# Performance work log

Hardware: AMD Instinct MI355X
Metric: run time of the kernel (lower is better)

The kernel has to match this reference:

```python
import jax, jax.numpy as jnp
import numpy as np

B, NS, S, H = 2048, 8, 8, 512   # batch, num_units, num_mem_slots, hidden==num_mem_size
WH, WK = 1, 32                  # write attention heads, key_size
RH, RK = 4, 32                  # read (mem) attention heads, mem_attention_key


def _lin(x, W, b):
    # torch nn.Linear convention: W is [out, in]
    return jnp.einsum('...i,oi->...o', x, W) + b


def setup_inputs() -> dict:
    key = jax.random.key(0)
    ks = jax.random.split(key, 13)
    def w(k, o, i):
        return jax.random.normal(k, (o, i), jnp.float32) * 0.02
    d = {
        'h_s': jax.random.normal(ks[0], (B, NS, H), jnp.float32),
        'mem': jax.random.normal(ks[1], (B, S, H), jnp.float32),
        'wq_w': w(ks[2], WH * WK, H), 'wq_b': jnp.zeros((WH * WK,), jnp.float32),
        'wk_w': w(ks[3], WH * WK, H), 'wk_b': jnp.zeros((WH * WK,), jnp.float32),
        'wv_w': w(ks[4], WH * H, H), 'wv_b': jnp.zeros((WH * H,), jnp.float32),
        'wo_w': w(ks[5], H, WH * H), 'wo_b': jnp.zeros((H,), jnp.float32),
        'ut_w': w(ks[6], H, H),      'ut_b': jnp.zeros((H,), jnp.float32),
        'ug_w': w(ks[7], 2 * H, H),  'ug_b': jnp.zeros((2 * H,), jnp.float32),
        'rq_w': w(ks[8], RH * RK, H), 'rq_b': jnp.zeros((RH * RK,), jnp.float32),
        'rk_w': w(ks[9], RH * RK, H), 'rk_b': jnp.zeros((RH * RK,), jnp.float32),
        'rv_w': w(ks[10], RH * H, H), 'rv_b': jnp.zeros((RH * H,), jnp.float32),
        'ro_w': w(ks[11], H, RH * H), 'ro_b': jnp.zeros((H,), jnp.float32),
    }
    return d


def _forward(h_s, mem, wq_w, wq_b, wk_w, wk_b, wv_w, wv_b, wo_w, wo_b,
             ut_w, ut_b, ug_w, ug_b, rq_w, rq_b, rk_w, rk_b, rv_w, rv_b,
             ro_w, ro_b):
    b = h_s.shape[0]
    T = NS + S  # concat length for write keys/values

    # ---------------- write ----------------
    xi = jnp.concatenate([h_s, mem], axis=1)                       # [B, T, H]
    q = _lin(mem, wq_w, wq_b).reshape(b, S, WH, WK).transpose(0, 2, 1, 3)   # [B,WH,S,WK]
    k = _lin(xi, wk_w, wk_b).reshape(b, T, WH, WK).transpose(0, 2, 1, 3)    # [B,WH,T,WK]
    v = _lin(xi, wv_w, wv_b).reshape(b, T, WH, H).transpose(0, 2, 1, 3)     # [B,WH,T,H]
    scores = jnp.einsum('bhsk,bhtk->bhst', q, k) / np.sqrt(WK).astype(np.float32)
    probs = jax.nn.softmax(scores, axis=-1)                         # [B,WH,S,T]
    ctx = jnp.einsum('bhst,bhtd->bhsd', probs, v)                   # [B,WH,S,H]
    ctx = ctx.transpose(0, 2, 1, 3).reshape(b, S, WH * H)
    mem_write = _lin(ctx, wo_w, wo_b)                               # [B,S,H]

    # ---------------- update (GRU-like gating) ----------------
    inputs_mean = jax.nn.relu(_lin(h_s, ut_w, ut_b)).mean(axis=1, keepdims=True)  # [B,1,H]
    kk = inputs_mean + jnp.tanh(mem)                                # [B,S,H]
    gates = jax.nn.sigmoid(_lin(kk, ug_w, ug_b))                    # [B,S,2H]
    input_gate, forget_gate = gates[..., :H], gates[..., H:]
    mem_new = input_gate * jnp.tanh(mem_write) + forget_gate * mem  # [B,S,H]

    # ---------------- read ----------------
    q = _lin(h_s, rq_w, rq_b).reshape(b, NS, RH, RK).transpose(0, 2, 1, 3)      # [B,RH,NS,RK]
    k = _lin(mem_new, rk_w, rk_b).reshape(b, S, RH, RK).transpose(0, 2, 1, 3)   # [B,RH,S,RK]
    v = _lin(mem_new, rv_w, rv_b).reshape(b, S, RH, H).transpose(0, 2, 1, 3)    # [B,RH,S,H]
    scores = jnp.einsum('bhnk,bhsk->bhns', q, k) / np.sqrt(RK).astype(np.float32)
    probs = jax.nn.softmax(scores, axis=-1)                          # [B,RH,NS,S]
    ctx = jnp.einsum('bhns,bhsd->bhnd', probs, v)                    # [B,RH,NS,H]
    ctx = ctx.transpose(0, 2, 1, 3).reshape(b, NS, RH * H)
    h_out = h_s + _lin(ctx, ro_w, ro_b)                              # residual
    return h_out, mem_new


def reference(h_s, mem, wq_w, wq_b, wk_w, wk_b, wv_w, wv_b, wo_w, wo_b,
              ut_w, ut_b, ug_w, ug_b, rq_w, rq_b, rk_w, rk_b, rv_w, rv_b,
              ro_w, ro_b):
    return _forward(h_s, mem, wq_w, wq_b, wk_w, wk_b, wv_w, wv_b, wo_w, wo_b,
                    ut_w, ut_b, ug_w, ug_b, rq_w, rq_b, rk_w, rk_b, rv_w, rv_b,
                    ro_w, ro_b)
```

## Files before the change

### kernel.cpp

```cpp
#include <hip/hip_runtime.h>

#define Bb   2048
#define Mrows 16384
#define Hd   512

typedef float  f32x4  __attribute__((ext_vector_type(4)));
typedef __bf16 bf16x8 __attribute__((ext_vector_type(8)));
typedef unsigned short us8 __attribute__((ext_vector_type(8)));

__device__ __forceinline__ unsigned short f2bf(float f) {
    unsigned int u = __builtin_bit_cast(unsigned int, f);
    u = u + 0x7FFFu + ((u >> 16) & 1u);
    return (unsigned short)(u >> 16);
}
__device__ __forceinline__ float bf2f(unsigned short h) {
    unsigned int u = ((unsigned int)h) << 16;
    return __builtin_bit_cast(float, u);
}

__device__ __forceinline__ void gload_lds16(const unsigned short* g, void* lds) {
    __builtin_amdgcn_global_load_lds(
        (const __attribute__((address_space(1))) unsigned int*)g,
        (__attribute__((address_space(3))) unsigned int*)lds,
        16, 0, 0);
}

#define MB (1024ull*1024ull)
#define OFF_WQ   0ull
#define OFF_WK   32768ull
#define OFF_WV   65536ull
#define OFF_WO   589824ull
#define OFF_UT   1114112ull
#define OFF_UG   1638400ull
#define OFF_RQ   2686976ull
#define OFF_RK   2818048ull
#define OFF_RV   2949120ull
#define OFF_RO   5046272ull
#define OFF_HS    (8*MB)
#define OFF_MEM   (24*MB)
#define OFF_UTR   (40*MB)
#define OFF_MEAN  (56*MB)
#define OFF_Q1    (60*MB)
#define OFF_K1    (62*MB)
#define OFF_V1    (66*MB)
#define OFF_CTX1  (100*MB)
#define OFF_KK    (116*MB)
#define OFF_TMW   (132*MB)
#define OFF_GATES (148*MB)
#define OFF_MNB   (180*MB)
#define OFF_Q2    (196*MB)
#define OFF_K2    (204*MB)
#define OFF_RVO   (40*MB)
#define OFF_CTX2  (104*MB)

struct CastSeg { const float* src; unsigned short* dst; int n4; };
struct CastParams { CastSeg seg[12]; };

__global__ __launch_bounds__(256) void cast_all(CastParams p) {
    CastSeg s = p.seg[blockIdx.y];
    int stride = gridDim.x * blockDim.x;
    for (int i = blockIdx.x * blockDim.x + threadIdx.x; i < s.n4; i += stride) {
        float4 v = reinterpret_cast<const float4*>(s.src)[i];
        ushort4 o;
        o.x = f2bf(v.x); o.y = f2bf(v.y); o.z = f2bf(v.z); o.w = f2bf(v.w);
        reinterpret_cast<ushort4*>(s.dst)[i] = o;
    }
}

template<int MODE>
__device__ __forceinline__ void store_c(void* out, const float* extra, int row,
                                        int col, int ldo, int remap_off, float v) {
    if (MODE == 0) {
        ((float*)out)[(size_t)row * ldo + col] = v;
    } else if (MODE == 1) {
        ((unsigned short*)out)[(size_t)row * ldo + col] = f2bf(v);
    } else if (MODE == 2) {
        ((unsigned short*)out)[(size_t)row * ldo + col] = f2bf(fmaxf(v, 0.f));
    } else if (MODE == 3) {
        ((unsigned short*)out)[(size_t)row * ldo + col] = f2bf(1.f / (1.f + expf(-v)));
    } else if (MODE == 4) {
        ((unsigned short*)out)[(size_t)row * ldo + col] = f2bf(tanhf(v));
    } else if (MODE == 5) {
        int rr = ((row >> 3) << 4) + (row & 7) + remap_off;
        ((float*)out)[(size_t)rr * ldo + col] = v;
    } else if (MODE == 6) {
        int rr = ((row >> 3) << 4) + (row & 7) + remap_off;
        ((unsigned short*)out)[(size_t)rr * ldo + col] = f2bf(v);
    } else if (MODE == 7) {
        ((float*)out)[(size_t)row * ldo + col] = v + extra[(size_t)row * ldo + col];
    }
}

struct GemmSeg {
    const unsigned short* A;
    const unsigned short* W;
    const float* bias;
    void* out;
    const float* extra;
    int mode, ldo, remap_off, tile0;
};
struct GemmParams { GemmSeg seg[4]; int nseg; int tiles_tot; };

template<int K>
__global__ __launch_bounds__(256, 2) void gemm_multi(GemmParams p)
{
    constexpr int NT = K / 64;
    __shared__ __align__(16) unsigned short As[2][128 * 64];
    __shared__ __align__(16) unsigned short Bs[2][128 * 64];

    const int nwg = (int)gridDim.x;
    const int swz = ((int)blockIdx.x & 7) * (nwg >> 3) + ((int)blockIdx.x >> 3);
    const int bm = swz / p.tiles_tot;
    const int tl = swz - bm * p.tiles_tot;

    int si = 0;
    #pragma unroll
    for (int i = 1; i < 4; i++)
        if (i < p.nseg && tl >= p.seg[i].tile0) si = i;
    const unsigned short* Aseg = p.seg[si].A;
    const unsigned short* Wseg = p.seg[si].W;
    const int bn = tl - p.seg[si].tile0;

    const int t = threadIdx.x;
    const int wave = t >> 6, lane = t & 63;
    const int wr = (wave >> 1) * 64;
    const int wc = (wave & 1) * 64;
    const int lrow = lane & 15;
    const int lkh  = lane >> 4;

    const unsigned short* ga[4];
    const unsigned short* gb[4];
    #pragma unroll
    for (int j = 0; j < 4; j++) {
        int c   = wave * 256 + j * 64 + lane;
        int row = c >> 3;
        int kl  = (c & 7) ^ (row & 7);
        ga[j] = Aseg + (size_t)(bm * 128 + row) * K + kl * 8;
        gb[j] = Wseg + (size_t)(bn * 128 + row) * K + kl * 8;
    }

    int aof[4][2], bof[4][2];
    #pragma unroll
    for (int m = 0; m < 4; m++) {
        int ra = wr + m * 16 + lrow;
        int rb = wc + m * 16 + lrow;
        #pragma unroll
        for (int kk = 0; kk < 2; kk++) {
            int kc = kk * 4 + lkh;
            aof[m][kk] = ra * 64 + ((kc ^ (ra & 7)) << 3);
            bof[m][kk] = rb * 64 + ((kc ^ (rb & 7)) << 3);
        }
    }

    f32x4 acc[4][4] = {};

    #pragma unroll
    for (int j = 0; j < 4; j++) {
        gload_lds16(ga[j], (char*)As[0] + (wave * 4 + j) * 1024);
        gload_lds16(gb[j], (char*)Bs[0] + (wave * 4 + j) * 1024);
    }
    __syncthreads();

    #pragma unroll 8
    for (int kt = 0; kt < NT; ++kt) {
        const int cur = kt & 1, nxt = cur ^ 1;
        if (kt + 1 < NT) {
            #pragma unroll
            for (int j = 0; j < 4; j++) {
                gload_lds16(ga[j] + (kt + 1) * 64, (char*)As[nxt] + (wave * 4 + j) * 1024);
                gload_lds16(gb[j] + (kt + 1) * 64, (char*)Bs[nxt] + (wave * 4 + j) * 1024);
            }
        }
        #pragma unroll
        for (int kk = 0; kk < 2; kk++) {
            bf16x8 af[4], bf_[4];
            #pragma unroll
            for (int m = 0; m < 4; m++)
                af[m] = __builtin_bit_cast(bf16x8,
                            *reinterpret_cast<const us8*>(&As[cur][aof[m][kk]]));
            #pragma unroll
            for (int n = 0; n < 4; n++)
                bf_[n] = __builtin_bit_cast(bf16x8,
                            *reinterpret_cast<const us8*>(&Bs[cur][bof[n][kk]]));
            #pragma unroll
            for (int m = 0; m < 4; m++)
                #pragma unroll
                for (int n = 0; n < 4; n++)
                    acc[m][n] = __builtin_amdgcn_mfma_f32_16x16x32_bf16(
                                    af[m], bf_[n], acc[m][n], 0, 0, 0);
        }
        __syncthreads();
    }

    void* outp = p.seg[si].out;
    const float* bias = p.seg[si].bias;
    const float* extra = p.seg[si].extra;
    const int ldo = p.seg[si].ldo, rmo = p.seg[si].remap_off, mode = p.seg[si].mode;

    #define EPI(MODE_)                                                          \
        _Pragma("unroll")                                                       \
        for (int n = 0; n < 4; n++) {                                           \
            int col = bn * 128 + wc + n * 16 + lrow;                            \
            float bv = bias[col];                                               \
            _Pragma("unroll")                                                   \
            for (int m = 0; m < 4; m++) {                                       \
                _Pragma("unroll")                                               \
                for (int r = 0; r < 4; r++) {                                   \
                    int row = bm * 128 + wr + m * 16 + lkh * 4 + r;             \
                    store_c<MODE_>(outp, extra, row, col, ldo, rmo,             \
                                   acc[m][n][r] + bv);                          \
                }                                                               \
            }                                                                   \
        }
    switch (mode) {
        case 0: EPI(0) break;
        case 1: EPI(1) break;
        case 2: EPI(2) break;
        case 3: EPI(3) break;
        case 4: EPI(4) break;
        case 5: EPI(5) break;
        case 6: EPI(6) break;
        default: EPI(7) break;
    }
    #undef EPI
}

template<int TN, int MODE, int K>
__global__ __launch_bounds__(256) void gemm_small(
    const unsigned short* __restrict__ A, const unsigned short* __restrict__ W,
    const float* __restrict__ bias, void* __restrict__ out,
    const float* __restrict__ extra, int N, int ldo, int remap_off)
{
    constexpr int BN = 16 * TN;
    const int tiles_n = N / BN;
    const int bm = blockIdx.x / tiles_n;
    const int bn = blockIdx.x % tiles_n;
    const int wave = threadIdx.x >> 6;
    const int lane = threadIdx.x & 63;
    const int row0 = bm * 64 + wave * 16;
    const int col0 = bn * BN;
    const int lrow = lane & 15;
    const int lk   = (lane >> 4) << 3;

    f32x4 acc[TN] = {};
    const unsigned short* ap  = A + (size_t)(row0 + lrow) * K + lk;
    const unsigned short* wp0 = W + (size_t)(col0 + lrow) * K + lk;

    #pragma unroll 4
    for (int ks = 0; ks < K; ks += 32) {
        bf16x8 af = __builtin_bit_cast(bf16x8,
                        *reinterpret_cast<const us8*>(ap + ks));
        #pragma unroll
        for (int tt = 0; tt < TN; tt++) {
            bf16x8 bfm = __builtin_bit_cast(bf16x8,
                        *reinterpret_cast<const us8*>(wp0 + (size_t)tt * 16 * K + ks));
            acc[tt] = __builtin_amdgcn_mfma_f32_16x16x32_bf16(af, bfm, acc[tt], 0, 0, 0);
        }
    }

    #pragma unroll
    for (int tt = 0; tt < TN; tt++) {
        int col = col0 + tt * 16 + lrow;
        float bv = bias[col];
        #pragma unroll
        for (int r = 0; r < 4; r++) {
            int row = row0 + (lane >> 4) * 4 + r;
            store_c<MODE>(out, extra, row, col, ldo, remap_off, acc[tt][r] + bv);
        }
    }
}

__global__ __launch_bounds__(256) void mean_kernel(
    const unsigned short* __restrict__ UTR, float* __restrict__ MEAN)
{
    int idx = blockIdx.x * blockDim.x + threadIdx.x;
    if (idx >= Bb * Hd) return;
    int b = idx >> 9, j = idx & 511;
    float s = 0.f;
    #pragma unroll
    for (int r = 0; r < 8; r++)
        s += bf2f(UTR[((size_t)(b * 8 + r) << 9) + j]);
    MEAN[idx] = s * 0.125f;
}

__global__ __launch_bounds__(256) void kk_kernel(
    const float* __restrict__ MEAN, const float* __restrict__ mem,
    unsigned short* __restrict__ KK)
{
    int idx = blockIdx.x * blockDim.x + threadIdx.x;
    int m = idx >> 9;
    int bj = ((m >> 3) << 9) + (idx & 511);
    KK[idx] = f2bf(MEAN[bj] + tanhf(mem[idx]));
}

__global__ __launch_bounds__(256) void memnew_kernel(
    const unsigned short* __restrict__ GATES, const unsigned short* __restrict__ TMW,
    const float* __restrict__ mem, float* __restrict__ out_mem,
    unsigned short* __restrict__ MNB)
{
    int idx = blockIdx.x * blockDim.x + threadIdx.x;
    int m = idx >> 9, j = idx & 511;
    float ig = bf2f(GATES[(size_t)m * 1024 + j]);
    float fg = bf2f(GATES[(size_t)m * 1024 + 512 + j]);
    float v  = ig * bf2f(TMW[idx]) + fg * mem[idx];
    out_mem[idx] = v;
    MNB[idx] = f2bf(v);
}

__global__ __launch_bounds__(256) void attn1_kernel(
    const float* __restrict__ Q1, const float* __restrict__ K1,
    const unsigned short* __restrict__ V1, unsigned short* __restrict__ CTX1)
{
    int b = blockIdx.x, t = threadIdx.x;
    __shared__ float q[8][32], k[16][32], pr[8][16];
    q[t >> 5][t & 31] = Q1[(size_t)b * 256 + t];
    k[t >> 5][t & 31]       = K1[(size_t)b * 512 + t];
    k[8 + (t >> 5)][t & 31] = K1[(size_t)b * 512 + 256 + t];
    __syncthreads();
    if (t < 128) {
        int s = t >> 4, tt = t & 15;
        float acc = 0.f;
        #pragma unroll
        for (int i = 0; i < 32; i++) acc += q[s][i] * k[tt][i];
        pr[s][tt] = acc * 0.17677669529663687f;
    }
    __syncthreads();
    if (t < 8) {
        float m = -1e30f;
        for (int i = 0; i < 16; i++) m = fmaxf(m, pr[t][i]);
        float e[16], sum = 0.f;
        for (int i = 0; i < 16; i++) { e[i] = expf(pr[t][i] - m); sum += e[i]; }
        float inv = 1.f / sum;
        for (int i = 0; i < 16; i++) pr[t][i] = e[i] * inv;
    }
    __syncthreads();
    int s = t >> 5, d0 = (t & 31) * 16;
    float a[16];
    #pragma unroll
    for (int i = 0; i < 16; i++) a[i] = 0.f;
    for (int tt = 0; tt < 16; tt++) {
        float p = pr[s][tt];
        const unsigned short* vp = V1 + ((size_t)(b * 16 + tt)) * 512 + d0;
        us8 v0 = *reinterpret_cast<const us8*>(vp);
        us8 v1 = *reinterpret_cast<const us8*>(vp + 8);
        #pragma unroll
        for (int i = 0; i < 8; i++) a[i]     += p * bf2f(v0[i]);
        #pragma unroll
        for (int i = 0; i < 8; i++) a[8 + i] += p * bf2f(v1[i]);
    }
    us8 o0, o1;
    #pragma unroll
    for (int i = 0; i < 8; i++) { o0[i] = f2bf(a[i]); o1[i] = f2bf(a[8 + i]); }
    unsigned short* cp = CTX1 + ((size_t)(b * 8 + s)) * 512 + d0;
    *reinterpret_cast<us8*>(cp) = o0;
    *reinterpret_cast<us8*>(cp + 8) = o1;
}

__global__ __launch_bounds__(256) void attn2_kernel(
    const float* __restrict__ Q2, const float* __restrict__ K2,
    const unsigned short* __restrict__ V2, unsigned short* __restrict__ CTX2)
{
    int b = blockIdx.x, t = threadIdx.x;
    __shared__ float q[8][128], k[8][128], pr[4][8][8];
    for (int i = t; i < 1024; i += 256) {
        q[i >> 7][i & 127] = Q2[(size_t)b * 1024 + i];
        k[i >> 7][i & 127] = K2[(size_t)b * 1024 + i];
    }
    __syncthreads();
    {
        int h = t >> 6, n = (t >> 3) & 7, s = t & 7;
        float acc = 0.f;
        #pragma unroll
        for (int i = 0; i < 32; i++) acc += q[n][h * 32 + i] * k[s][h * 32 + i];
        pr[h][n][s] = acc * 0.17677669529663687f;
    }
    __syncthreads();
    if (t < 32) {
        int h = t >> 3, n = t & 7;
        float m = -1e30f;
        for (int i = 0; i < 8; i++) m = fmaxf(m, pr[h][n][i]);
        float e[8], sum = 0.f;
        for (int i = 0; i < 8; i++) { e[i] = expf(pr[h][n][i] - m); sum += e[i]; }
        float inv = 1.f / sum;
        for (int i = 0; i < 8; i++) pr[h][n][i] = e[i] * inv;
    }
    __syncthreads();
    int n = t >> 5, d0 = (t & 31) * 16;
    for (int h = 0; h < 4; h++) {
        float a[16];
        #pragma unroll
        for (int i = 0; i < 16; i++) a[i] = 0.f;
        for (int s = 0; s < 8; s++) {
            float p = pr[h][n][s];
            const unsigned short* vp = V2 + ((size_t)(b * 8 + s)) * 2048 + h * 512 + d0;
            us8 v0 = *reinterpret_cast<const us8*>(vp);
            us8 v1 = *reinterpret_cast<const us8*>(vp + 8);
            #pragma unroll
            for (int i = 0; i < 8; i++) a[i]     += p * bf2f(v0[i]);
            #pragma unroll
            for (int i = 0; i < 8; i++) a[8 + i] += p * bf2f(v1[i]);
        }
        us8 o0, o1;
        #pragma unroll
        for (int i = 0; i < 8; i++) { o0[i] = f2bf(a[i]); o1[i] = f2bf(a[8 + i]); }
        unsigned short* cp = CTX2 + ((size_t)(b * 8 + n)) * 2048 + h * 512 + d0;
        *reinterpret_cast<us8*>(cp) = o0;
        *reinterpret_cast<us8*>(cp + 8) = o1;
    }
}

extern "C" void kernel_launch(void* const* d_in, const int* in_sizes, int n_in,
                              void* d_out, int out_size, void* d_ws, size_t ws_size,
                              hipStream_t stream)
{
    const float* h_s  = (const float*)d_in[0];
    const float* mem  = (const float*)d_in[1];
    const float* wq_w = (const float*)d_in[2];  const float* wq_b = (const float*)d_in[3];
    const float* wk_w = (const float*)d_in[4];  const float* wk_b = (const float*)d_in[5];
    const float* wv_w = (const float*)d_in[6];  const float* wv_b = (const float*)d_in[7];
    const float* wo_w = (const float*)d_in[8];  const float* wo_b = (const float*)d_in[9];
    const float* ut_w = (const float*)d_in[10]; const float* ut_b = (const float*)d_in[11];
    const float* ug_w = (const float*)d_in[12]; const float* ug_b = (const float*)d_in[13];
    const float* rq_w = (const float*)d_in[14]; const float* rq_b = (const float*)d_in[15];
    const float* rk_w = (const float*)d_in[16]; const float* rk_b = (const float*)d_in[17];
    const float* rv_w = (const float*)d_in[18]; const float* rv_b = (const float*)d_in[19];
    const float* ro_w = (const float*)d_in[20]; const float* ro_b = (const float*)d_in[21];

    char* ws = (char*)d_ws;
    unsigned short* WQb = (unsigned short*)(ws + OFF_WQ);
    unsigned short* WKb = (unsigned short*)(ws + OFF_WK);
    unsigned short* WVb = (unsigned short*)(ws + OFF_WV);
    unsigned short* WOb = (unsigned short*)(ws + OFF_WO);
    unsigned short* UTb = (unsigned short*)(ws + OFF_UT);
    unsigned short* UGb = (unsigned short*)(ws + OFF_UG);
    unsigned short* RQb = (unsigned short*)(ws + OFF_RQ);
    unsigned short* RKb = (unsigned short*)(ws + OFF_RK);
    unsigned short* RVb = (unsigned short*)(ws + OFF_RV);
    unsigned short* ROb = (unsigned short*)(ws + OFF_RO);
    unsigned short* HSb  = (unsigned short*)(ws + OFF_HS);
    unsigned short* MEMb = (unsigned short*)(ws + OFF_MEM);
    unsigned short* UTR  = (unsigned short*)(ws + OFF_UTR);
    float*          MEAN = (float*)(ws + OFF_MEAN);
    float*          Q1   = (float*)(ws + OFF_Q1);
    float*          K1   = (float*)(ws + OFF_K1);
    unsigned short* V1   = (unsigned short*)(ws + OFF_V1);
    unsigned short* CTX1 = (unsigned short*)(ws + OFF_CTX1);
    unsigned short* KKb  = (unsigned short*)(ws + OFF_KK);
    unsigned short* TMW  = (unsigned short*)(ws + OFF_TMW);
    unsigned short* GATES= (unsigned short*)(ws + OFF_GATES);
    unsigned short* MNB  = (unsigned short*)(ws + OFF_MNB);
    float*          Q2   = (float*)(ws + OFF_Q2);
    float*          K2   = (float*)(ws + OFF_K2);
    unsigned short* RVO  = (unsigned short*)(ws + OFF_RVO);
    unsigned short* CTX2 = (unsigned short*)(ws + OFF_CTX2);

    float* out   = (float*)d_out;
    float* out_m = out + (size_t)Mrows * Hd;

    CastParams cp;
    cp.seg[0]  = { h_s,  HSb,  (Mrows * Hd) / 4 };
    cp.seg[1]  = { mem,  MEMb, (Mrows * Hd) / 4 };
    cp.seg[2]  = { wq_w, WQb,  (32 * 512) / 4 };
    cp.seg[3]  = { wk_w, WKb,  (32 * 512) / 4 };
    cp.seg[4]  = { wv_w, WVb,  (512 * 512) / 4 };
    cp.seg[5]  = { wo_w, WOb,  (512 * 512) / 4 };
    cp.seg[6]  = { ut_w, UTb,  (512 * 512) / 4 };
    cp.seg[7]  = { ug_w, UGb,  (1024 * 512) / 4 };
    cp.seg[8]  = { rq_w, RQb,  (128 * 512) / 4 };
    cp.seg[9]  = { rk_w, RKb,  (128 * 512) / 4 };
    cp.seg[10] = { rv_w, RVb,  (2048 * 512) / 4 };
    cp.seg[11] = { ro_w, ROb,  (512 * 2048) / 4 };
    cast_all<<<dim3(2048, 12), 256, 0, stream>>>(cp);

    {
        GemmParams g;
        g.seg[0] = { HSb,  UTb, ut_b, UTR, nullptr, 2, 512,  0, 0 };
        g.seg[1] = { HSb,  WVb, wv_b, V1,  nullptr, 6, 512,  0, 4 };
        g.seg[2] = { HSb,  RQb, rq_b, Q2,  nullptr, 0, 128,  0, 8 };
        g.seg[3] = { MEMb, WVb, wv_b, V1,  nullptr, 6, 512,  8, 9 };
        g.nseg = 4; g.tiles_tot = 13;
        gemm_multi<512><<<128 * 13, 256, 0, stream>>>(g);
    }
    gemm_small<2,5,512><<<256, 256, 0, stream>>>(HSb,  WKb, wk_b, K1, nullptr, 32, 32, 0);
    gemm_small<2,0,512><<<256, 256, 0, stream>>>(MEMb, WQb, wq_b, Q1, nullptr, 32, 32, 0);
    gemm_small<2,5,512><<<256, 256, 0, stream>>>(MEMb, WKb, wk_b, K1, nullptr, 32, 32, 8);

    mean_kernel<<<4096, 256, 0, stream>>>(UTR, MEAN);
    kk_kernel<<<32768, 256, 0, stream>>>(MEAN, mem, KKb);

    attn1_kernel<<<Bb, 256, 0, stream>>>(Q1, K1, V1, CTX1);

    {
        GemmParams g;
        g.seg[0] = { CTX1, WOb, wo_b, TMW,   nullptr, 4,  512, 0, 0 };
        g.seg[1] = { KKb,  UGb, ug_b, GATES, nullptr, 3, 1024, 0, 4 };
        g.nseg = 2; g.tiles_tot = 12;
        gemm_multi<512><<<128 * 12, 256, 0, stream>>>(g);
    }

    memnew_kernel<<<32768, 256, 0, stream>>>(GATES, TMW, mem, out_m, MNB);

    {
        GemmParams g;
        g.seg[0] = { MNB, RKb, rk_b, K2,  nullptr, 0,  128, 0, 0 };
        g.seg[1] = { MNB, RVb, rv_b, RVO, nullptr, 1, 2048, 0, 1 };
        g.nseg = 2; g.tiles_tot = 17;
        gemm_multi<512><<<128 * 17, 256, 0, stream>>>(g);
    }

    attn2_kernel<<<Bb, 256, 0, stream>>>(Q2, K2, RVO, CTX2);

    {
        GemmParams g;
        g.seg[0] = { CTX2, ROb, ro_b, out, h_s, 7, 512, 0, 0 };
        g.nseg = 1; g.tiles_tot = 4;
        gemm_multi<2048><<<128 * 4, 256, 0, stream>>>(g);
    }

    (void)in_sizes; (void)n_in; (void)out_size; (void)ws_size;
}
```

Measured before the change: 532.5 us.

## Shrink GEMM K-tile, merge small GEMMs, fuse mean/kk, vectorize memnew

The main GEMM now uses a 32-wide K tile with half the LDS, which permits 4 workgroups per CU, and its loop is restructured around an explicit vmcnt wait and barrier at the top of each iteration. The three tiny N=32 GEMMs are combined into one launch. The mean and kk elementwise kernels are fused so the mean stays in registers instead of round-tripping through global memory. memnew is vectorized to 4 elements per thread. The aim is fewer launches, less memory traffic and higher occupancy, at the cost of more barriers per K in the GEMM.

```diff
diff --git a/kernel.cpp b/kernel.cpp
--- a/kernel.cpp
+++ b/kernel.cpp
@@ -39,7 +39,6 @@
 #define OFF_HS    (8*MB)
 #define OFF_MEM   (24*MB)
 #define OFF_UTR   (40*MB)
-#define OFF_MEAN  (56*MB)
 #define OFF_Q1    (60*MB)
 #define OFF_K1    (62*MB)
 #define OFF_V1    (66*MB)
@@ -102,11 +101,11 @@
 struct GemmParams { GemmSeg seg[4]; int nseg; int tiles_tot; };
 
 template<int K>
-__global__ __launch_bounds__(256, 2) void gemm_multi(GemmParams p)
-{
-    constexpr int NT = K / 64;
-    __shared__ __align__(16) unsigned short As[2][128 * 64];
-    __shared__ __align__(16) unsigned short Bs[2][128 * 64];
+__global__ __launch_bounds__(256, 4) void gemm_multi(GemmParams p)
+{
+    constexpr int NT = K / 32;
+    __shared__ __align__(16) unsigned short As[2][128 * 32];
+    __shared__ __align__(16) unsigned short Bs[2][128 * 32];
 
     const int nwg = (int)gridDim.x;
     const int swz = ((int)blockIdx.x & 7) * (nwg >> 3) + ((int)blockIdx.x >> 3);
@@ -128,68 +127,62 @@
     const int lrow = lane & 15;
     const int lkh  = lane >> 4;
 
-    const unsigned short* ga[4];
-    const unsigned short* gb[4];
-    #pragma unroll
-    for (int j = 0; j < 4; j++) {
-        int c   = wave * 256 + j * 64 + lane;
-        int row = c >> 3;
-        int kl  = (c & 7) ^ (row & 7);
+    const unsigned short* ga[2];
+    const unsigned short* gb[2];
+    #pragma unroll
+    for (int j = 0; j < 2; j++) {
+        int c   = wave * 128 + j * 64 + lane;
+        int row = c >> 2;
+        int kl  = (c & 3) ^ (row & 3);
         ga[j] = Aseg + (size_t)(bm * 128 + row) * K + kl * 8;
         gb[j] = Wseg + (size_t)(bn * 128 + row) * K + kl * 8;
     }
 
-    int aof[4][2], bof[4][2];
+    int aof[4], bof[4];
     #pragma unroll
     for (int m = 0; m < 4; m++) {
         int ra = wr + m * 16 + lrow;
         int rb = wc + m * 16 + lrow;
-        #pragma unroll
-        for (int kk = 0; kk < 2; kk++) {
-            int kc = kk * 4 + lkh;
-            aof[m][kk] = ra * 64 + ((kc ^ (ra & 7)) << 3);
-            bof[m][kk] = rb * 64 + ((kc ^ (rb & 7)) << 3);
-        }
+        aof[m] = ra * 32 + ((lkh ^ (ra & 3)) << 3);
+        bof[m] = rb * 32 + ((lkh ^ (rb & 3)) << 3);
     }
 
     f32x4 acc[4][4] = {};
 
     #pragma unroll
-    for (int j = 0; j < 4; j++) {
-        gload_lds16(ga[j], (char*)As[0] + (wave * 4 + j) * 1024);
-        gload_lds16(gb[j], (char*)Bs[0] + (wave * 4 + j) * 1024);
-    }
-    __syncthreads();
-
-    #pragma unroll 8
+    for (int j = 0; j < 2; j++) {
+        gload_lds16(ga[j], (char*)As[0] + (wave * 2 + j) * 1024);
+        gload_lds16(gb[j], (char*)Bs[0] + (wave * 2 + j) * 1024);
+    }
+
+    #pragma unroll 2
     for (int kt = 0; kt < NT; ++kt) {
-        const int cur = kt & 1, nxt = cur ^ 1;
+        const int cur = kt & 1;
+        asm volatile("s_waitcnt vmcnt(0)" ::: "memory");
+        __builtin_amdgcn_s_barrier();
+        __builtin_amdgcn_sched_barrier(0);
         if (kt + 1 < NT) {
             #pragma unroll
-            for (int j = 0; j < 4; j++) {
-                gload_lds16(ga[j] + (kt + 1) * 64, (char*)As[nxt] + (wave * 4 + j) * 1024);
-                gload_lds16(gb[j] + (kt + 1) * 64, (char*)Bs[nxt] + (wave * 4 + j) * 1024);
+            for (int j = 0; j < 2; j++) {
+                gload_lds16(ga[j] + (kt + 1) * 32, (char*)As[cur ^ 1] + (wave * 2 + j) * 1024);
+                gload_lds16(gb[j] + (kt + 1) * 32, (char*)Bs[cur ^ 1] + (wave * 2 + j) * 1024);
             }
         }
-        #pragma unroll
-        for (int kk = 0; kk < 2; kk++) {
-            bf16x8 af[4], bf_[4];
-            #pragma unroll
-            for (int m = 0; m < 4; m++)
-                af[m] = __builtin_bit_cast(bf16x8,
-                            *reinterpret_cast<const us8*>(&As[cur][aof[m][kk]]));
+        bf16x8 af[4], bfr[4];
+        #pragma unroll
+        for (int m = 0; m < 4; m++)
+            af[m] = __builtin_bit_cast(bf16x8,
+                        *reinterpret_cast<const us8*>(&As[cur][aof[m]]));
+        #pragma unroll
+        for (int n = 0; n < 4; n++)
+            bfr[n] = __builtin_bit_cast(bf16x8,
+                        *reinterpret_cast<const us8*>(&Bs[cur][bof[n]]));
+        #pragma unroll
+        for (int m = 0; m < 4; m++)
             #pragma unroll
             for (int n = 0; n < 4; n++)
-                bf_[n] = __builtin_bit_cast(bf16x8,
-                            *reinterpret_cast<const us8*>(&Bs[cur][bof[n][kk]]));
-            #pragma unroll
-            for (int m = 0; m < 4; m++)
-                #pragma unroll
-                for (int n = 0; n < 4; n++)
-                    acc[m][n] = __builtin_amdgcn_mfma_f32_16x16x32_bf16(
-                                    af[m], bf_[n], acc[m][n], 0, 0, 0);
-        }
-        __syncthreads();
+                acc[m][n] = __builtin_amdgcn_mfma_f32_16x16x32_bf16(
+                                af[m], bfr[n], acc[m][n], 0, 0, 0);
     }
 
     void* outp = p.seg[si].out;
@@ -225,33 +218,38 @@
     #undef EPI
 }
 
-template<int TN, int MODE, int K>
-__global__ __launch_bounds__(256) void gemm_small(
-    const unsigned short* __restrict__ A, const unsigned short* __restrict__ W,
-    const float* __restrict__ bias, void* __restrict__ out,
-    const float* __restrict__ extra, int N, int ldo, int remap_off)
-{
-    constexpr int BN = 16 * TN;
-    const int tiles_n = N / BN;
-    const int bm = blockIdx.x / tiles_n;
-    const int bn = blockIdx.x % tiles_n;
+struct SmallSeg {
+    const unsigned short* A;
+    const unsigned short* W;
+    const float* bias;
+    float* out;
+    int mode, remap_off;
+};
+struct SmallParams { SmallSeg seg[3]; };
+
+__global__ __launch_bounds__(256) void gemm_small3(SmallParams p)
+{
+    constexpr int K = 512;
+    const int si = blockIdx.x >> 8;
+    const int bm = blockIdx.x & 255;
+    const SmallSeg s = p.seg[si];
+
     const int wave = threadIdx.x >> 6;
     const int lane = threadIdx.x & 63;
     const int row0 = bm * 64 + wave * 16;
-    const int col0 = bn * BN;
     const int lrow = lane & 15;
     const int lk   = (lane >> 4) << 3;
 
-    f32x4 acc[TN] = {};
-    const unsigned short* ap  = A + (size_t)(row0 + lrow) * K + lk;
-    const unsigned short* wp0 = W + (size_t)(col0 + lrow) * K + lk;
+    f32x4 acc[2] = {};
+    const unsigned short* ap  = s.A + (size_t)(row0 + lrow) * K + lk;
+    const unsigned short* wp0 = s.W + (size_t)lrow * K + lk;
 
     #pragma unroll 4
     for (int ks = 0; ks < K; ks += 32) {
         bf16x8 af = __builtin_bit_cast(bf16x8,
                         *reinterpret_cast<const us8*>(ap + ks));
         #pragma unroll
-        for (int tt = 0; tt < TN; tt++) {
+        for (int tt = 0; tt < 2; tt++) {
             bf16x8 bfm = __builtin_bit_cast(bf16x8,
                         *reinterpret_cast<const us8*>(wp0 + (size_t)tt * 16 * K + ks));
             acc[tt] = __builtin_amdgcn_mfma_f32_16x16x32_bf16(af, bfm, acc[tt], 0, 0, 0);
@@ -259,38 +257,42 @@
     }
 
     #pragma unroll
-    for (int tt = 0; tt < TN; tt++) {
-        int col = col0 + tt * 16 + lrow;
-        float bv = bias[col];
+    for (int tt = 0; tt < 2; tt++) {
+        int col = tt * 16 + lrow;
+        float bv = s.bias[col];
         #pragma unroll
         for (int r = 0; r < 4; r++) {
             int row = row0 + (lane >> 4) * 4 + r;
-            store_c<MODE>(out, extra, row, col, ldo, remap_off, acc[tt][r] + bv);
+            float v = acc[tt][r] + bv;
+            if (s.mode == 0) {
+                s.out[(size_t)row * 32 + col] = v;
+            } else {
+                int rr = ((row >> 3) << 4) + (row & 7) + s.remap_off;
+                s.out[(size_t)rr * 32 + col] = v;
+            }
         }
     }
 }
 
-__global__ __launch_bounds__(256) void mean_kernel(
-    const unsigned short* __restrict__ UTR, float* __restrict__ MEAN)
-{
-    int idx = blockIdx.x * blockDim.x + threadIdx.x;
-    if (idx >= Bb * Hd) return;
-    int b = idx >> 9, j = idx & 511;
-    float s = 0.f;
-    #pragma unroll
-    for (int r = 0; r < 8; r++)
-        s += bf2f(UTR[((size_t)(b * 8 + r) << 9) + j]);
-    MEAN[idx] = s * 0.125f;
-}
-
-__global__ __launch_bounds__(256) void kk_kernel(
-    const float* __restrict__ MEAN, const float* __restrict__ mem,
+__global__ __launch_bounds__(256) void meankk_kernel(
+    const unsigned short* __restrict__ UTR, const float* __restrict__ mem,
     unsigned short* __restrict__ KK)
 {
-    int idx = blockIdx.x * blockDim.x + threadIdx.x;
-    int m = idx >> 9;
-    int bj = ((m >> 3) << 9) + (idx & 511);
-    KK[idx] = f2bf(MEAN[bj] + tanhf(mem[idx]));
+    int b = blockIdx.x;
+    #pragma unroll
+    for (int half = 0; half < 2; half++) {
+        int j = threadIdx.x + half * 256;
+        float sum = 0.f;
+        #pragma unroll
+        for (int r = 0; r < 8; r++)
+            sum += bf2f(UTR[((size_t)(b * 8 + r) << 9) + j]);
+        float mn = sum * 0.125f;
+        #pragma unroll
+        for (int r = 0; r < 8; r++) {
+            size_t idx = ((size_t)(b * 8 + r) << 9) + j;
+            KK[idx] = f2bf(mn + tanhf(mem[idx]));
+        }
+    }
 }
 
 __global__ __launch_bounds__(256) void memnew_kernel(
@@ -298,13 +300,20 @@
     const float* __restrict__ mem, float* __restrict__ out_mem,
     unsigned short* __restrict__ MNB)
 {
-    int idx = blockIdx.x * blockDim.x + threadIdx.x;
-    int m = idx >> 9, j = idx & 511;
-    float ig = bf2f(GATES[(size_t)m * 1024 + j]);
-    float fg = bf2f(GATES[(size_t)m * 1024 + 512 + j]);
-    float v  = ig * bf2f(TMW[idx]) + fg * mem[idx];
-    out_mem[idx] = v;
-    MNB[idx] = f2bf(v);
+    int idx = blockIdx.x * 256 + threadIdx.x;
+    int m = idx >> 7, j4 = idx & 127;
+    ushort4 ig4 = reinterpret_cast<const ushort4*>(GATES + (size_t)m * 1024)[j4];
+    ushort4 fg4 = reinterpret_cast<const ushort4*>(GATES + (size_t)m * 1024 + 512)[j4];
+    ushort4 tm4 = reinterpret_cast<const ushort4*>(TMW + (size_t)m * 512)[j4];
+    float4  mm  = reinterpret_cast<const float4*>(mem + (size_t)m * 512)[j4];
+    float4 v;
+    v.x = bf2f(ig4.x) * bf2f(tm4.x) + bf2f(fg4.x) * mm.x;
+    v.y = bf2f(ig4.y) * bf2f(tm4.y) + bf2f(fg4.y) * mm.y;
+    v.z = bf2f(ig4.z) * bf2f(tm4.z) + bf2f(fg4.z) * mm.z;
+    v.w = bf2f(ig4.w) * bf2f(tm4.w) + bf2f(fg4.w) * mm.w;
+    reinterpret_cast<float4*>(out_mem + (size_t)m * 512)[j4] = v;
+    ushort4 o; o.x = f2bf(v.x); o.y = f2bf(v.y); o.z = f2bf(v.z); o.w = f2bf(v.w);
+    reinterpret_cast<ushort4*>(MNB + (size_t)m * 512)[j4] = o;
 }
 
 __global__ __launch_bounds__(256) void attn1_kernel(
@@ -440,7 +449,6 @@
     unsigned short* HSb  = (unsigned short*)(ws + OFF_HS);
     unsigned short* MEMb = (unsigned short*)(ws + OFF_MEM);
     unsigned short* UTR  = (unsigned short*)(ws + OFF_UTR);
-    float*          MEAN = (float*)(ws + OFF_MEAN);
     float*          Q1   = (float*)(ws + OFF_Q1);
     float*          K1   = (float*)(ws + OFF_K1);
     unsigned short* V1   = (unsigned short*)(ws + OFF_V1);
@@ -481,12 +489,15 @@
         g.nseg = 4; g.tiles_tot = 13;
         gemm_multi<512><<<128 * 13, 256, 0, stream>>>(g);
     }
-    gemm_small<2,5,512><<<256, 256, 0, stream>>>(HSb,  WKb, wk_b, K1, nullptr, 32, 32, 0);
-    gemm_small<2,0,512><<<256, 256, 0, stream>>>(MEMb, WQb, wq_b, Q1, nullptr, 32, 32, 0);
-    gemm_small<2,5,512><<<256, 256, 0, stream>>>(MEMb, WKb, wk_b, K1, nullptr, 32, 32, 8);
-
-    mean_kernel<<<4096, 256, 0, stream>>>(UTR, MEAN);
-    kk_kernel<<<32768, 256, 0, stream>>>(MEAN, mem, KKb);
+    {
+        SmallParams sp;
+        sp.seg[0] = { HSb,  WKb, wk_b, K1, 5, 0 };
+        sp.seg[1] = { MEMb, WQb, wq_b, Q1, 0, 0 };
+        sp.seg[2] = { MEMb, WKb, wk_b, K1, 5, 8 };
+        gemm_small3<<<768, 256, 0, stream>>>(sp);
+    }
+
+    meankk_kernel<<<Bb, 256, 0, stream>>>(UTR, mem, KKb);
 
     attn1_kernel<<<Bb, 256, 0, stream>>>(Q1, K1, V1, CTX1);
 
@@ -498,7 +509,7 @@
         gemm_multi<512><<<128 * 12, 256, 0, stream>>>(g);
     }
 
-    memnew_kernel<<<32768, 256, 0, stream>>>(GATES, TMW, mem, out_m, MNB);
+    memnew_kernel<<<8192, 256, 0, stream>>>(GATES, TMW, mem, out_m, MNB);
 
     {
         GemmParams g;
```

New measurement: 524.5 us. About the same (-1.5%).
